# Kernel optimization log

Measured on AMD Instinct MI355X. Metric: run time of the kernel, lower is better.

The kernel has to match this reference:

```python
import jax, jax.numpy as jnp
import numpy as np

N_NODES = 10000
N_EDGES = 160000
C = 128          # hidden_channels
H = 8            # heads
G = 16           # groups
L_LAYERS = 5
NUM_FEAT = 14
DIM_OUT = 16
CH = C // H      # channels per head (16)


def setup_inputs() -> dict:
    key = jax.random.key(0)
    ks = jax.random.split(key, 12)
    inp = {
        "x": jax.random.normal(ks[0], (N_NODES, NUM_FEAT), dtype=jnp.float32),
        "edge_index": jax.random.randint(ks[1], (2, N_EDGES), 0, N_NODES, dtype=jnp.int64),
        "lin1_w": jax.random.normal(ks[2], (NUM_FEAT, C), dtype=jnp.float32) * 0.1,
        "lin1_b": jax.random.normal(ks[3], (C,), dtype=jnp.float32) * 0.1,
        "Wq": jax.random.normal(ks[4], (L_LAYERS, G, C // G, C // G), dtype=jnp.float32) * 0.1,
        "bq": jax.random.normal(ks[5], (L_LAYERS, C), dtype=jnp.float32) * 0.1,
        "Wk": jax.random.normal(ks[6], (L_LAYERS, G, C // G, C // G), dtype=jnp.float32) * 0.1,
        "bk": jax.random.normal(ks[7], (L_LAYERS, C), dtype=jnp.float32) * 0.1,
        "Wv": jax.random.normal(ks[8], (L_LAYERS, G, C // G, C // G), dtype=jnp.float32) * 0.1,
        "bv": jax.random.normal(ks[9], (L_LAYERS, C), dtype=jnp.float32) * 0.1,
        "lin2_w": jax.random.normal(ks[10], (C, DIM_OUT), dtype=jnp.float32) * 0.1,
        "lin2_b": jax.random.normal(ks[11], (DIM_OUT,), dtype=jnp.float32) * 0.1,
    }
    return inp


def _grouped_linear(z, W, b):
    # z: [..., C]; W: [G, C/G, C/G]; b: [C]  (PyG grouped Linear)
    lead = z.shape[:-1]
    zg = z.reshape(lead + (G, C // G))
    out = jnp.einsum('...gi,gio->...go', zg, W)
    return out.reshape(lead + (C,)) + b


def _dna_forward(x, edge_index, lin1_w, lin1_b, Wq, bq, Wk, bk, Wv, bv, lin2_w, lin2_b):
    n = x.shape[0]
    # gcn_norm with self-loops (edge_weight = 1)
    loops = jnp.arange(n, dtype=edge_index.dtype)
    row = jnp.concatenate([edge_index[0], loops])  # sources (x_j)
    col = jnp.concatenate([edge_index[1], loops])  # targets (x_i, aggregation)
    ew = jnp.ones(row.shape[0], dtype=x.dtype)
    deg = jax.ops.segment_sum(ew, col, num_segments=n)
    dis = jax.lax.rsqrt(deg)  # deg >= 1 due to self-loops
    norm = dis[row] * dis[col]  # [Et]

    h = jax.nn.relu(x @ lin1_w + lin1_b)  # [N, C]
    x_all = h[:, None, :]                  # [N, 1, C]

    scale = 1.0 / np.sqrt(CH).astype(np.float32)
    for l in range(L_LAYERS):
        q = _grouped_linear(x_all[col, -1], Wq[l], bq[l])   # [Et, C]
        k = _grouped_linear(x_all[row], Wk[l], bk[l])       # [Et, L, C]
        v = _grouped_linear(x_all[row], Wv[l], bv[l])       # [Et, L, C]
        Et, Lh = k.shape[0], k.shape[1]
        qh = q.reshape(Et, H, CH)
        kh = k.reshape(Et, Lh, H, CH)
        vh = v.reshape(Et, Lh, H, CH)
        score = jnp.einsum('ehc,elhc->ehl', qh, kh) * scale
        attn = jax.nn.softmax(score, axis=-1)
        out = jnp.einsum('ehl,elhc->ehc', attn, vh).reshape(Et, C)
        msg = norm[:, None] * out
        agg = jax.ops.segment_sum(msg, col, num_segments=n)  # [N, C]
        xl = jax.nn.relu(agg)
        x_all = jnp.concatenate([x_all, xl[:, None, :]], axis=1)

    return x_all[:, -1] @ lin2_w + lin2_b  # [N, dim]


def reference(x, edge_index, lin1_w, lin1_b, Wq, bq, Wk, bk, Wv, bv, lin2_w, lin2_b):
    return _dna_forward(x, edge_index, lin1_w, lin1_b, Wq, bq, Wk, bk, Wv, bv,
                        lin2_w, lin2_b)
```

## Files before the change

kernel.cpp:

```cpp
#include <hip/hip_runtime.h>

#define N_NODES 10000
#define N_EDGESN 160000
#define E_TOT   (N_EDGESN + N_NODES)
#define C 128
#define H 8
#define G 16
#define LLAYERS 5
#define NUM_FEAT 14
#define DIM_OUT 16
#define CH 16
#define CG 8
#define XSTRIDE (6*C)
#define X16STRIDE (6*C)

typedef _Float16 half8 __attribute__((ext_vector_type(8)));
typedef _Float16 half2v __attribute__((ext_vector_type(2)));

__global__ void k_zero(int* __restrict__ counts) {
    int i = blockIdx.x * blockDim.x + threadIdx.x;
    if (i < N_NODES) counts[i] = 1;
}

__global__ void k_count(const int* __restrict__ col, int* __restrict__ counts) {
    int e = blockIdx.x * blockDim.x + threadIdx.x;
    if (e < N_EDGESN) atomicAdd(&counts[col[e]], 1);
}

__global__ __launch_bounds__(1024) void k_scan(const int* __restrict__ counts,
                                               int* __restrict__ offs, int* __restrict__ cursor,
                                               float* __restrict__ dis) {
    __shared__ int part[1024];
    const int CHK = (N_NODES + 1023) / 1024;
    int t = threadIdx.x;
    int base = t * CHK;
    int loc[CHK];
    int sum = 0;
#pragma unroll
    for (int i = 0; i < CHK; i++) {
        int idx = base + i;
        int v = (idx < N_NODES) ? counts[idx] : 0;
        loc[i] = sum;
        sum += v;
    }
    part[t] = sum;
    __syncthreads();
    for (int off = 1; off < 1024; off <<= 1) {
        int v = (t >= off) ? part[t - off] : 0;
        __syncthreads();
        part[t] += v;
        __syncthreads();
    }
    int prev = (t > 0) ? part[t - 1] : 0;
#pragma unroll
    for (int i = 0; i < CHK; i++) {
        int idx = base + i;
        if (idx < N_NODES) {
            int o = prev + loc[i];
            offs[idx] = o;
            cursor[idx] = o;
            dis[idx] = rsqrtf((float)counts[idx]);
        }
    }
    if (t == 1023) offs[N_NODES] = part[1023];
}

__global__ void k_scatter(const int* __restrict__ row, const int* __restrict__ col,
                          const float* __restrict__ dis,
                          int* __restrict__ cursor, int2* __restrict__ csr) {
    int e = blockIdx.x * blockDim.x + threadIdx.x;
    if (e >= E_TOT) return;
    int r = (e < N_EDGESN) ? row[e] : (e - N_EDGESN);
    int c = (e < N_EDGESN) ? col[e] : (e - N_EDGESN);
    int pos = atomicAdd(&cursor[c], 1);
    int2 pay;
    pay.x = r;
    pay.y = __float_as_int(dis[r]);
    csr[pos] = pay;
}

__global__ __launch_bounds__(256) void k_lin1(const float* __restrict__ x,
                                              const float* __restrict__ w,
                                              const float* __restrict__ b,
                                              float* __restrict__ x_all,
                                              _Float16* __restrict__ x16) {
    __shared__ float sw[NUM_FEAT * C];
    __shared__ float sb[C];
    int tid = threadIdx.x;
    for (int i = tid; i < NUM_FEAT * C; i += 256) sw[i] = w[i];
    if (tid < C) sb[tid] = b[tid];
    __syncthreads();
    int node = blockIdx.x * 2 + tid / C;
    int c = tid & (C - 1);
    if (node >= N_NODES) return;
    const float* xr = x + node * NUM_FEAT;
    float acc = sb[c];
#pragma unroll
    for (int f = 0; f < NUM_FEAT; f++) acc += xr[f] * sw[f * C + c];
    acc = fmaxf(acc, 0.0f);
    x_all[node * XSTRIDE + c] = acc;
    x16[(size_t)node * X16STRIDE + c] = (_Float16)acc;
}

__device__ __forceinline__ float dot8v(const float4& a, const float4& b,
                                       const float4& wa, const float4& wb) {
    return a.x * wa.x + a.y * wa.y + a.z * wa.z + a.w * wa.w
         + b.x * wb.x + b.y * wb.y + b.z * wb.z + b.w * wb.w;
}

template <int NL>
__global__ __launch_bounds__(256) void k_attn_fly(const int* __restrict__ offs,
                                                  const int2* __restrict__ csr,
                                                  const float* __restrict__ dis,
                                                  const float* __restrict__ Wq, const float* __restrict__ bq,
                                                  const float* __restrict__ Wk, const float* __restrict__ bk,
                                                  const float* __restrict__ Wv, const float* __restrict__ bv,
                                                  float* __restrict__ x_all,
                                                  _Float16* __restrict__ x16) {
    const int l = NL - 1;
    int w = threadIdx.x >> 6;
    int lane = threadIdx.x & 63;
    int d = blockIdx.x * 4 + w;
    if (d >= N_NODES) return;
    int g = lane >> 2;
    int j4 = lane & 3;
    int c0 = 2 * lane;
    int o0 = 2 * j4;

    float y8[8];
    float z = 0.f;
    if constexpr (NL > 1) {
        const float* xq = x_all + (size_t)d * XSTRIDE + l * C + 8 * g;
        float4 xda = *(const float4*)xq;
        float4 xdb = *(const float4*)(xq + 4);
        const float* bqg = bq + l * C + 8 * g;
        float4 qa = *(const float4*)bqg;
        float4 qb = *(const float4*)(bqg + 4);
        const float* wq = Wq + l * (G * CG * CG) + g * (CG * CG);
        float xdv[8] = {xda.x, xda.y, xda.z, xda.w, xdb.x, xdb.y, xdb.z, xdb.w};
#pragma unroll
        for (int i = 0; i < 8; i++) {
            float4 ra = *(const float4*)(wq + i * CG);
            float4 rb = *(const float4*)(wq + i * CG + 4);
            qa.x += xdv[i] * ra.x; qa.y += xdv[i] * ra.y;
            qa.z += xdv[i] * ra.z; qa.w += xdv[i] * ra.w;
            qb.x += xdv[i] * rb.x; qb.y += xdv[i] * rb.y;
            qb.z += xdv[i] * rb.z; qb.w += xdv[i] * rb.w;
        }
        const float* wk = Wk + l * (G * CG * CG) + g * (CG * CG);
#pragma unroll
        for (int j = 0; j < 8; j++) {
            float4 ra = *(const float4*)(wk + j * CG);
            float4 rb = *(const float4*)(wk + j * CG + 4);
            y8[j] = dot8v(qa, qb, ra, rb);
        }
        const float* bkg = bk + l * C + 8 * g;
        z = dot8v(qa, qb, *(const float4*)bkg, *(const float4*)(bkg + 4));
    }

    const float disd = dis[d];
    const int p0 = offs[d], p1 = offs[d + 1];
    const float scale = 0.25f;
    float xacc[8] = {0.f, 0.f, 0.f, 0.f, 0.f, 0.f, 0.f, 0.f};
    float nsum = 0.f;

    if constexpr (NL == 1) {
        for (int p = p0 + j4; p < p1; p += 4) {
            int2 pay = csr[p];
            float nrm = disd * __int_as_float(pay.y);
            const _Float16* xs = x16 + (size_t)pay.x * X16STRIDE + 8 * g;
            half8 hv = *(const half8*)xs;
#pragma unroll
            for (int i = 0; i < 8; i++) xacc[i] += nrm * (float)hv[i];
            nsum += nrm;
        }
    } else {
        auto consume = [&](int2 pay, const half8 (&buf)[NL]) {
            float nrm = disd * __int_as_float(pay.y);
            float xv[NL][8];
            float sc[NL];
#pragma unroll
            for (int t = 0; t < NL; t++) {
#pragma unroll
                for (int i = 0; i < 8; i++) xv[t][i] = (float)buf[t][i];
                float part = z;
#pragma unroll
                for (int i = 0; i < 8; i++) part += xv[t][i] * y8[i];
                part += __shfl_xor(part, 4);
                sc[t] = part * scale;
            }
            float mx = sc[0];
#pragma unroll
            for (int t = 1; t < NL; t++) mx = fmaxf(mx, sc[t]);
            float s = 0.f;
            float ex[8] = {0.f, 0.f, 0.f, 0.f, 0.f, 0.f, 0.f, 0.f};
#pragma unroll
            for (int t = 0; t < NL; t++) {
                float e = __expf(sc[t] - mx);
                s += e;
#pragma unroll
                for (int i = 0; i < 8; i++) ex[i] += e * xv[t][i];
            }
            float inv = nrm * __builtin_amdgcn_rcpf(s);
#pragma unroll
            for (int i = 0; i < 8; i++) xacc[i] += inv * ex[i];
            nsum += nrm;
        };

        int p = p0 + j4;
        if (p < p1) {
            int2 payA = csr[p];
            half8 bufA[NL];
            {
                const _Float16* xs = x16 + (size_t)payA.x * X16STRIDE + 8 * g;
#pragma unroll
                for (int t = 0; t < NL; t++) bufA[t] = *(const half8*)(xs + t * C);
            }
            int pn = p + 4;
            int2 payB = csr[(pn < p1) ? pn : p];
            for (; pn < p1; pn += 4) {
                half8 bufB[NL];
                const _Float16* xs = x16 + (size_t)payB.x * X16STRIDE + 8 * g;
#pragma unroll
                for (int t = 0; t < NL; t++) bufB[t] = *(const half8*)(xs + t * C);
                int pc = pn + 4;
                int2 payC = csr[(pc < p1) ? pc : p0];
                consume(payA, bufA);
                payA = payB;
                payB = payC;
#pragma unroll
                for (int t = 0; t < NL; t++) bufA[t] = bufB[t];
            }
            consume(payA, bufA);
        }
    }

#pragma unroll
    for (int i = 0; i < 8; i++) {
        xacc[i] += __shfl_xor(xacc[i], 1);
        xacc[i] += __shfl_xor(xacc[i], 2);
    }
    nsum += __shfl_xor(nsum, 1);
    nsum += __shfl_xor(nsum, 2);

    const float* wv = Wv + l * (G * CG * CG) + g * (CG * CG);
    float a0 = bv[l * C + c0] * nsum;
    float a1 = bv[l * C + c0 + 1] * nsum;
#pragma unroll
    for (int i = 0; i < 8; i++) {
        a0 += xacc[i] * wv[i * CG + o0];
        a1 += xacc[i] * wv[i * CG + o0 + 1];
    }
    a0 = fmaxf(a0, 0.f);
    a1 = fmaxf(a1, 0.f);
    float2 vo = make_float2(a0, a1);
    *(float2*)(x_all + (size_t)d * XSTRIDE + (l + 1) * C + c0) = vo;
    half2v ho;
    ho[0] = (_Float16)a0;
    ho[1] = (_Float16)a1;
    *(half2v*)(x16 + (size_t)d * X16STRIDE + (l + 1) * C + c0) = ho;
}

__global__ __launch_bounds__(256) void k_lin2(const float* __restrict__ x_all,
                                              const float* __restrict__ w,
                                              const float* __restrict__ b,
                                              float* __restrict__ out) {
    __shared__ float sw[C * DIM_OUT];
    __shared__ float sb[DIM_OUT];
    __shared__ float sx[16][C];
    int tid = threadIdx.x;
    for (int i = tid; i < C * DIM_OUT; i += 256) sw[i] = w[i];
    if (tid < DIM_OUT) sb[tid] = b[tid];
    int node0 = blockIdx.x * 16;
    for (int i = tid; i < 16 * C; i += 256) {
        int nn = node0 + i / C;
        sx[i / C][i & (C - 1)] = (nn < N_NODES) ? x_all[(size_t)nn * XSTRIDE + 5 * C + (i & (C - 1))] : 0.0f;
    }
    __syncthreads();
    int node = node0 + tid / DIM_OUT;
    int o = tid & (DIM_OUT - 1);
    if (node >= N_NODES) return;
    float acc = sb[o];
    const float* xr = sx[tid / DIM_OUT];
#pragma unroll 8
    for (int c = 0; c < C; c++) acc += xr[c] * sw[c * DIM_OUT + o];
    out[node * DIM_OUT + o] = acc;
}

extern "C" void kernel_launch(void* const* d_in, const int* in_sizes, int n_in,
                              void* d_out, int out_size, void* d_ws, size_t ws_size,
                              hipStream_t stream) {
    const float* x      = (const float*)d_in[0];
    const int*   edge   = (const int*)d_in[1];
    const int*   row    = edge;
    const int*   col    = edge + N_EDGESN;
    const float* lin1_w = (const float*)d_in[2];
    const float* lin1_b = (const float*)d_in[3];
    const float* Wq     = (const float*)d_in[4];
    const float* bq     = (const float*)d_in[5];
    const float* Wk     = (const float*)d_in[6];
    const float* bk     = (const float*)d_in[7];
    const float* Wv     = (const float*)d_in[8];
    const float* bv     = (const float*)d_in[9];
    const float* lin2_w = (const float*)d_in[10];
    const float* lin2_b = (const float*)d_in[11];
    float* outp = (float*)d_out;

    float*     ws    = (float*)d_ws;
    float*     x_all = ws;
    _Float16*  x16   = (_Float16*)(x_all + (size_t)N_NODES * XSTRIDE);
    float*     dis   = (float*)(x16 + (size_t)N_NODES * X16STRIDE);
    int*   counts = (int*)(dis + N_NODES);
    int*   offs   = counts + N_NODES;
    int*   cursor = offs + N_NODES + 1;
    int2*  csr    = (int2*)(cursor + N_NODES);

    k_zero<<<(N_NODES + 255) / 256, 256, 0, stream>>>(counts);
    k_count<<<(N_EDGESN + 255) / 256, 256, 0, stream>>>(col, counts);
    k_scan<<<1, 1024, 0, stream>>>(counts, offs, cursor, dis);
    k_scatter<<<(E_TOT + 255) / 256, 256, 0, stream>>>(row, col, dis, cursor, csr);
    k_lin1<<<N_NODES / 2, 256, 0, stream>>>(x, lin1_w, lin1_b, x_all, x16);

    const int ablocks = (N_NODES + 3) / 4;
    for (int l = 0; l < LLAYERS; l++) {
        switch (l) {
            case 0: k_attn_fly<1><<<ablocks, 256, 0, stream>>>(offs, csr, dis, Wq, bq, Wk, bk, Wv, bv, x_all, x16); break;
            case 1: k_attn_fly<2><<<ablocks, 256, 0, stream>>>(offs, csr, dis, Wq, bq, Wk, bk, Wv, bv, x_all, x16); break;
            case 2: k_attn_fly<3><<<ablocks, 256, 0, stream>>>(offs, csr, dis, Wq, bq, Wk, bk, Wv, bv, x_all, x16); break;
            case 3: k_attn_fly<4><<<ablocks, 256, 0, stream>>>(offs, csr, dis, Wq, bq, Wk, bk, Wv, bv, x_all, x16); break;
            case 4: k_attn_fly<5><<<ablocks, 256, 0, stream>>>(offs, csr, dis, Wq, bq, Wk, bk, Wv, bv, x_all, x16); break;
        }
    }
    k_lin2<<<(N_NODES + 15) / 16, 256, 0, stream>>>(x_all, lin2_w, lin2_b, outp);
}
```

Baseline: 231.4 us.

## Drop fp32 feature copy, fuse zeroing into lin1, and sort nodes by degree

Removes the fp32 x_all buffer entirely, so the query input and lin2 now read the fp16 copy, which cuts memory writes and reads per layer. The k_zero launch is folded into k_lin1. k_scan now builds a degree histogram and k_scatter a degree-sorted node permutation (largest first), which the attention kernels use to pick node order and so balance wavefront load. The cost is lower precision on the query input and final features, plus a few extra atomics during setup.

Result: slower. 242.2 us (+4.7%).

```diff
diff --git a/kernel.cpp b/kernel.cpp
--- a/kernel.cpp
+++ b/kernel.cpp
@@ -11,15 +11,33 @@
 #define DIM_OUT 16
 #define CH 16
 #define CG 8
-#define XSTRIDE (6*C)
 #define X16STRIDE (6*C)
 
 typedef _Float16 half8 __attribute__((ext_vector_type(8)));
 typedef _Float16 half2v __attribute__((ext_vector_type(2)));
 
-__global__ void k_zero(int* __restrict__ counts) {
-    int i = blockIdx.x * blockDim.x + threadIdx.x;
-    if (i < N_NODES) counts[i] = 1;
+__global__ __launch_bounds__(256) void k_lin1(const float* __restrict__ x,
+                                              const float* __restrict__ w,
+                                              const float* __restrict__ b,
+                                              _Float16* __restrict__ x16,
+                                              int* __restrict__ counts) {
+    __shared__ float sw[NUM_FEAT * C];
+    __shared__ float sb[C];
+    int tid = threadIdx.x;
+    int gid = blockIdx.x * 256 + tid;
+    if (gid < N_NODES) counts[gid] = 0;
+    for (int i = tid; i < NUM_FEAT * C; i += 256) sw[i] = w[i];
+    if (tid < C) sb[tid] = b[tid];
+    __syncthreads();
+    int node = blockIdx.x * 2 + tid / C;
+    int c = tid & (C - 1);
+    if (node >= N_NODES) return;
+    const float* xr = x + node * NUM_FEAT;
+    float acc = sb[c];
+#pragma unroll
+    for (int f = 0; f < NUM_FEAT; f++) acc += xr[f] * sw[f * C + c];
+    acc = fmaxf(acc, 0.0f);
+    x16[(size_t)node * X16STRIDE + c] = (_Float16)acc;
 }
 
 __global__ void k_count(const int* __restrict__ col, int* __restrict__ counts) {
@@ -29,19 +47,24 @@
 
 __global__ __launch_bounds__(1024) void k_scan(const int* __restrict__ counts,
                                                int* __restrict__ offs, int* __restrict__ cursor,
-                                               float* __restrict__ dis) {
+                                               float* __restrict__ dis,
+                                               int* __restrict__ bucket_cur) {
     __shared__ int part[1024];
+    __shared__ int hist[256];
     const int CHK = (N_NODES + 1023) / 1024;
     int t = threadIdx.x;
+    if (t < 256) hist[t] = 0;
+    __syncthreads();
     int base = t * CHK;
     int loc[CHK];
     int sum = 0;
 #pragma unroll
     for (int i = 0; i < CHK; i++) {
         int idx = base + i;
-        int v = (idx < N_NODES) ? counts[idx] : 0;
+        int v = (idx < N_NODES) ? (counts[idx] + 1) : 0;
         loc[i] = sum;
         sum += v;
+        if (idx < N_NODES) atomicAdd(&hist[min(v, 255)], 1);
     }
     part[t] = sum;
     __syncthreads();
@@ -59,16 +82,29 @@
             int o = prev + loc[i];
             offs[idx] = o;
             cursor[idx] = o;
-            dis[idx] = rsqrtf((float)counts[idx]);
+            dis[idx] = rsqrtf((float)(counts[idx] + 1));
         }
     }
     if (t == 1023) offs[N_NODES] = part[1023];
+    __syncthreads();
+    if (t == 0) {
+        int acc = 0;
+        for (int d2 = 255; d2 >= 0; d2--) { int h = hist[d2]; hist[d2] = acc; acc += h; }
+    }
+    __syncthreads();
+    if (t < 256) bucket_cur[t] = hist[t];
 }
 
 __global__ void k_scatter(const int* __restrict__ row, const int* __restrict__ col,
-                          const float* __restrict__ dis,
-                          int* __restrict__ cursor, int2* __restrict__ csr) {
+                          const float* __restrict__ dis, const int* __restrict__ counts,
+                          int* __restrict__ cursor, int2* __restrict__ csr,
+                          int* __restrict__ bucket_cur, int* __restrict__ perm) {
     int e = blockIdx.x * blockDim.x + threadIdx.x;
+    if (e < N_NODES) {
+        int deg = min(counts[e] + 1, 255);
+        int pos = atomicAdd(&bucket_cur[deg], 1);
+        perm[pos] = e;
+    }
     if (e >= E_TOT) return;
     int r = (e < N_EDGESN) ? row[e] : (e - N_EDGESN);
     int c = (e < N_EDGESN) ? col[e] : (e - N_EDGESN);
@@ -79,49 +115,19 @@
     csr[pos] = pay;
 }
 
-__global__ __launch_bounds__(256) void k_lin1(const float* __restrict__ x,
-                                              const float* __restrict__ w,
-                                              const float* __restrict__ b,
-                                              float* __restrict__ x_all,
-                                              _Float16* __restrict__ x16) {
-    __shared__ float sw[NUM_FEAT * C];
-    __shared__ float sb[C];
-    int tid = threadIdx.x;
-    for (int i = tid; i < NUM_FEAT * C; i += 256) sw[i] = w[i];
-    if (tid < C) sb[tid] = b[tid];
-    __syncthreads();
-    int node = blockIdx.x * 2 + tid / C;
-    int c = tid & (C - 1);
-    if (node >= N_NODES) return;
-    const float* xr = x + node * NUM_FEAT;
-    float acc = sb[c];
-#pragma unroll
-    for (int f = 0; f < NUM_FEAT; f++) acc += xr[f] * sw[f * C + c];
-    acc = fmaxf(acc, 0.0f);
-    x_all[node * XSTRIDE + c] = acc;
-    x16[(size_t)node * X16STRIDE + c] = (_Float16)acc;
-}
-
-__device__ __forceinline__ float dot8v(const float4& a, const float4& b,
-                                       const float4& wa, const float4& wb) {
-    return a.x * wa.x + a.y * wa.y + a.z * wa.z + a.w * wa.w
-         + b.x * wb.x + b.y * wb.y + b.z * wb.z + b.w * wb.w;
-}
-
 template <int NL>
 __global__ __launch_bounds__(256) void k_attn_fly(const int* __restrict__ offs,
                                                   const int2* __restrict__ csr,
                                                   const float* __restrict__ dis,
+                                                  const int* __restrict__ perm,
                                                   const float* __restrict__ Wq, const float* __restrict__ bq,
                                                   const float* __restrict__ Wk, const float* __restrict__ bk,
                                                   const float* __restrict__ Wv, const float* __restrict__ bv,
-                                                  float* __restrict__ x_all,
                                                   _Float16* __restrict__ x16) {
     const int l = NL - 1;
     int w = threadIdx.x >> 6;
     int lane = threadIdx.x & 63;
-    int d = blockIdx.x * 4 + w;
-    if (d >= N_NODES) return;
+    int d = perm[blockIdx.x * 4 + w];
     int g = lane >> 2;
     int j4 = lane & 3;
     int c0 = 2 * lane;
@@ -130,14 +136,14 @@
     float y8[8];
     float z = 0.f;
     if constexpr (NL > 1) {
-        const float* xq = x_all + (size_t)d * XSTRIDE + l * C + 8 * g;
-        float4 xda = *(const float4*)xq;
-        float4 xdb = *(const float4*)(xq + 4);
+        half8 hq = *(const half8*)(x16 + (size_t)d * X16STRIDE + l * C + 8 * g);
+        float xdv[8];
+#pragma unroll
+        for (int i = 0; i < 8; i++) xdv[i] = (float)hq[i];
         const float* bqg = bq + l * C + 8 * g;
         float4 qa = *(const float4*)bqg;
         float4 qb = *(const float4*)(bqg + 4);
         const float* wq = Wq + l * (G * CG * CG) + g * (CG * CG);
-        float xdv[8] = {xda.x, xda.y, xda.z, xda.w, xdb.x, xdb.y, xdb.z, xdb.w};
 #pragma unroll
         for (int i = 0; i < 8; i++) {
             float4 ra = *(const float4*)(wq + i * CG);
@@ -152,10 +158,14 @@
         for (int j = 0; j < 8; j++) {
             float4 ra = *(const float4*)(wk + j * CG);
             float4 rb = *(const float4*)(wk + j * CG + 4);
-            y8[j] = dot8v(qa, qb, ra, rb);
+            y8[j] = qa.x * ra.x + qa.y * ra.y + qa.z * ra.z + qa.w * ra.w
+                  + qb.x * rb.x + qb.y * rb.y + qb.z * rb.z + qb.w * rb.w;
         }
         const float* bkg = bk + l * C + 8 * g;
-        z = dot8v(qa, qb, *(const float4*)bkg, *(const float4*)(bkg + 4));
+        float4 ba = *(const float4*)bkg;
+        float4 bb = *(const float4*)(bkg + 4);
+        z = qa.x * ba.x + qa.y * ba.y + qa.z * ba.z + qa.w * ba.w
+          + qb.x * bb.x + qb.y * bb.y + qb.z * bb.z + qb.w * bb.w;
     }
 
     const float disd = dis[d];
@@ -168,8 +178,7 @@
         for (int p = p0 + j4; p < p1; p += 4) {
             int2 pay = csr[p];
             float nrm = disd * __int_as_float(pay.y);
-            const _Float16* xs = x16 + (size_t)pay.x * X16STRIDE + 8 * g;
-            half8 hv = *(const half8*)xs;
+            half8 hv = *(const half8*)(x16 + (size_t)pay.x * X16STRIDE + 8 * g);
 #pragma unroll
             for (int i = 0; i < 8; i++) xacc[i] += nrm * (float)hv[i];
             nsum += nrm;
@@ -253,15 +262,13 @@
     }
     a0 = fmaxf(a0, 0.f);
     a1 = fmaxf(a1, 0.f);
-    float2 vo = make_float2(a0, a1);
-    *(float2*)(x_all + (size_t)d * XSTRIDE + (l + 1) * C + c0) = vo;
     half2v ho;
     ho[0] = (_Float16)a0;
     ho[1] = (_Float16)a1;
     *(half2v*)(x16 + (size_t)d * X16STRIDE + (l + 1) * C + c0) = ho;
 }
 
-__global__ __launch_bounds__(256) void k_lin2(const float* __restrict__ x_all,
+__global__ __launch_bounds__(256) void k_lin2(const _Float16* __restrict__ x16,
                                               const float* __restrict__ w,
                                               const float* __restrict__ b,
                                               float* __restrict__ out) {
@@ -272,9 +279,17 @@
     for (int i = tid; i < C * DIM_OUT; i += 256) sw[i] = w[i];
     if (tid < DIM_OUT) sb[tid] = b[tid];
     int node0 = blockIdx.x * 16;
-    for (int i = tid; i < 16 * C; i += 256) {
-        int nn = node0 + i / C;
-        sx[i / C][i & (C - 1)] = (nn < N_NODES) ? x_all[(size_t)nn * XSTRIDE + 5 * C + (i & (C - 1))] : 0.0f;
+    {
+        int nn = node0 + (tid >> 4);
+        int co = (tid & 15) * 8;
+        if (nn < N_NODES) {
+            half8 hv = *(const half8*)(x16 + (size_t)nn * X16STRIDE + 5 * C + co);
+#pragma unroll
+            for (int i = 0; i < 8; i++) sx[tid >> 4][co + i] = (float)hv[i];
+        } else {
+#pragma unroll
+            for (int i = 0; i < 8; i++) sx[tid >> 4][co + i] = 0.f;
+        }
     }
     __syncthreads();
     int node = node0 + tid / DIM_OUT;
@@ -306,30 +321,29 @@
     const float* lin2_b = (const float*)d_in[11];
     float* outp = (float*)d_out;
 
-    float*     ws    = (float*)d_ws;
-    float*     x_all = ws;
-    _Float16*  x16   = (_Float16*)(x_all + (size_t)N_NODES * XSTRIDE);
-    float*     dis   = (float*)(x16 + (size_t)N_NODES * X16STRIDE);
+    _Float16* x16   = (_Float16*)d_ws;
+    int2*     csr   = (int2*)(x16 + (size_t)N_NODES * X16STRIDE);
+    float*    dis   = (float*)(csr + E_TOT);
     int*   counts = (int*)(dis + N_NODES);
     int*   offs   = counts + N_NODES;
     int*   cursor = offs + N_NODES + 1;
-    int2*  csr    = (int2*)(cursor + N_NODES);
-
-    k_zero<<<(N_NODES + 255) / 256, 256, 0, stream>>>(counts);
+    int*   bucket_cur = cursor + N_NODES;
+    int*   perm   = bucket_cur + 256;
+
+    k_lin1<<<N_NODES / 2, 256, 0, stream>>>(x, lin1_w, lin1_b, x16, counts);
     k_count<<<(N_EDGESN + 255) / 256, 256, 0, stream>>>(col, counts);
-    k_scan<<<1, 1024, 0, stream>>>(counts, offs, cursor, dis);
-    k_scatter<<<(E_TOT + 255) / 256, 256, 0, stream>>>(row, col, dis, cursor, csr);
-    k_lin1<<<N_NODES / 2, 256, 0, stream>>>(x, lin1_w, lin1_b, x_all, x16);
-
-    const int ablocks = (N_NODES + 3) / 4;
+    k_scan<<<1, 1024, 0, stream>>>(counts, offs, cursor, dis, bucket_cur);
+    k_scatter<<<(E_TOT + 255) / 256, 256, 0, stream>>>(row, col, dis, counts, cursor, csr, bucket_cur, perm);
+
+    const int ablocks = N_NODES / 4;
     for (int l = 0; l < LLAYERS; l++) {
         switch (l) {
-            case 0: k_attn_fly<1><<<ablocks, 256, 0, stream>>>(offs, csr, dis, Wq, bq, Wk, bk, Wv, bv, x_all, x16); break;
-            case 1: k_attn_fly<2><<<ablocks, 256, 0, stream>>>(offs, csr, dis, Wq, bq, Wk, bk, Wv, bv, x_all, x16); break;
-            case 2: k_attn_fly<3><<<ablocks, 256, 0, stream>>>(offs, csr, dis, Wq, bq, Wk, bk, Wv, bv, x_all, x16); break;
-            case 3: k_attn_fly<4><<<ablocks, 256, 0, stream>>>(offs, csr, dis, Wq, bq, Wk, bk, Wv, bv, x_all, x16); break;
-            case 4: k_attn_fly<5><<<ablocks, 256, 0, stream>>>(offs, csr, dis, Wq, bq, Wk, bk, Wv, bv, x_all, x16); break;
-        }
-    }
-    k_lin2<<<(N_NODES + 15) / 16, 256, 0, stream>>>(x_all, lin2_w, lin2_b, outp);
-}
+            case 0: k_attn_fly<1><<<ablocks, 256, 0, stream>>>(offs, csr, dis, perm, Wq, bq, Wk, bk, Wv, bv, x16); break;
+            case 1: k_attn_fly<2><<<ablocks, 256, 0, stream>>>(offs, csr, dis, perm, Wq, bq, Wk, bk, Wv, bv, x16); break;
+            case 2: k_attn_fly<3><<<ablocks, 256, 0, stream>>>(offs, csr, dis, perm, Wq, bq, Wk, bk, Wv, bv, x16); break;
+            case 3: k_attn_fly<4><<<ablocks, 256, 0, stream>>>(offs, csr, dis, perm, Wq, bq, Wk, bk, Wv, bv, x16); break;
+            case 4: k_attn_fly<5><<<ablocks, 256, 0, stream>>>(offs, csr, dis, perm, Wq, bq, Wk, bk, Wv, bv, x16); break;
+        }
+    }
+    k_lin2<<<(N_NODES + 15) / 16, 256, 0, stream>>>(x16, lin2_w, lin2_b, outp);
+}
```
